# Kernel optimization log

Measured on AMD Instinct MI355X. Metric: run time of the kernel, lower is better.

## Reference

```python
import math
import jax, jax.numpy as jnp
import numpy as np

TREE_DEPTH = 4
NUM_NODES = (1 << TREE_DEPTH) - 1  # 15
TAU_MEM = 0.95
TAU_SYN = 0.95
LN_EPS = 1e-5


def _forward(x, W_proj, threshold, node_weights, gamma, beta):
    B, T, D = x.shape
    padded_T = 1 << math.ceil(math.log2(T))
    x_p = jnp.pad(x, ((0, 0), (0, padded_T - T), (0, 0))) if padded_T > T else x

    eff_depth = min(TREE_DEPTH, int(math.log2(padded_T)))
    num_leaves = 1 << eff_depth
    sub_seq = padded_T // num_leaves
    # leaf states: mean over each contiguous chunk -> [B, num_leaves, D]
    leaves = x_p.reshape(B, num_leaves, sub_seq, D).mean(axis=2)

    leaf_start = (1 << (eff_depth - 1)) - 1
    valid_leaves = min(num_leaves, NUM_NODES - leaf_start)
    node_states = jnp.zeros((B, NUM_NODES, D), x.dtype)
    node_states = node_states.at[:, leaf_start:leaf_start + valid_leaves].set(
        leaves[:, :valid_leaves])

    # LIF membrane/synapse buffers, carried across levels within this forward
    v = jnp.zeros((1, 1, D), x.dtype)
    s = jnp.zeros((1, 1, D), x.dtype)

    # bottom-up tree message passing (static, unrolled: eff_depth levels)
    for level in range(eff_depth - 1, -1, -1):
        level_start = (1 << level) - 1
        level_end = min((1 << (level + 1)) - 1, NUM_NODES)
        nodes = np.arange(level_start, level_end)
        left = 2 * nodes + 1
        right = 2 * nodes + 2
        mask = left < NUM_NODES
        if not mask.any():
            continue  # leaf level: children out of range
        nv, lv, rv = nodes[mask], left[mask], right[mask]
        l_st = node_states[:, lv]   # [B, n, D]
        r_st = node_states[:, rv]   # [B, n, D] (full tree -> rv always valid)
        fused = jnp.concatenate([l_st, r_st], axis=-1)  # [B, n, 2D]
        proj = jnp.einsum('bnk,dk->bnd', fused, W_proj)

        # LIF neuron (training-mode math: surrogate * hard spike)
        s_new = TAU_SYN * s + proj                      # broadcast [B,n,D]
        v_new = TAU_MEM * v + s_new - jax.lax.stop_gradient(s_new)
        spike = (v_new >= threshold).astype(x.dtype)
        v_after = v_new - spike * threshold
        surrogate = jax.nn.sigmoid(25.0 * (v_after - threshold))
        spike_out = surrogate * spike
        v = jax.lax.stop_gradient(v_after.mean(axis=(0, 1), keepdims=True))
        s = jax.lax.stop_gradient(s_new.mean(axis=(0, 1), keepdims=True))

        gated = proj * spike_out
        node_states = node_states.at[:, nv].set(gated)

    # per-dim softmax mixture over the 15 tree nodes
    weights = jax.nn.softmax(node_weights, axis=0)             # [N, D]
    mixture = jnp.einsum('nd,bnd->bd', weights, node_states)   # [B, D]

    out = mixture[:, None, :] + x                              # residual, [B,T,D]
    mu = out.mean(axis=-1, keepdims=True)
    var = out.var(axis=-1, keepdims=True)
    out = (out - mu) / jnp.sqrt(var + LN_EPS) * gamma + beta
    return out


def setup_inputs() -> dict:
    key = jax.random.key(0)
    k0, k1, k2 = jax.random.split(key, 3)
    B, T, D = 8, 4096, 1024
    x = jax.random.normal(k0, (B, T, D), dtype=jnp.float32)
    # nn.Linear(2D, D, bias=False): weight [D, 2D]
    W_proj = jax.random.normal(k1, (D, 2 * D), dtype=jnp.float32) / np.sqrt(2 * D).astype(np.float32)
    threshold = jnp.ones((D,), dtype=jnp.float32)        # LIF init: ones
    node_weights = 0.02 * jax.random.normal(k2, (NUM_NODES, D), dtype=jnp.float32)
    gamma = jnp.ones((D,), dtype=jnp.float32)
    beta = jnp.zeros((D,), dtype=jnp.float32)
    return {"x": x, "W_proj": W_proj, "threshold": threshold,
            "node_weights": node_weights, "gamma": gamma, "beta": beta}


def reference(x, W_proj, threshold, node_weights, gamma, beta):
    return _forward(x, W_proj, threshold, node_weights, gamma, beta)
```

## Files before the change

### kernel.cpp

```cpp
#include <hip/hip_runtime.h>

#define Bq 8
#define Tq 4096
#define Dq 1024
#define NLEAF 8
#define SUBSEQ 256
#define TSPLIT 16
#define NNODES 15

typedef float f32x4 __attribute__((ext_vector_type(4)));

__global__ __launch_bounds__(256) void k_leaf_partial(const float* __restrict__ x,
                                                      float* __restrict__ partial) {
    const int bl = blockIdx.x;
    const int p  = blockIdx.y;
    const int q  = threadIdx.x;
    const int b = bl >> 3, l = bl & 7;
    const float4* xp = (const float4*)(x + ((size_t)b * Tq + (size_t)l * SUBSEQ + (size_t)p * (SUBSEQ / TSPLIT)) * Dq) + q;
    float4 s = {0.f, 0.f, 0.f, 0.f};
#pragma unroll
    for (int t = 0; t < SUBSEQ / TSPLIT; ++t) {
        float4 xv = xp[(size_t)t * (Dq / 4)];
        s.x += xv.x; s.y += xv.y; s.z += xv.z; s.w += xv.w;
    }
    ((float4*)partial)[((size_t)bl * TSPLIT + p) * (Dq / 4) + q] = s;
}

__global__ __launch_bounds__(256) void k_mixture(const float* __restrict__ partial,
                                                 const float* __restrict__ nw,
                                                 float* __restrict__ mixture) {
    const int b = blockIdx.x;
    const int d = blockIdx.y * 256 + threadIdx.x;
    float v[NNODES];
    float m = -1e30f;
#pragma unroll
    for (int n = 0; n < NNODES; ++n) {
        v[n] = nw[n * Dq + d];
        m = fmaxf(m, v[n]);
    }
    float denom = 0.f;
#pragma unroll
    for (int n = 0; n < NNODES; ++n) {
        v[n] = expf(v[n] - m);
        denom += v[n];
    }
    const float inv_denom = 1.0f / denom;
    float acc = 0.f;
#pragma unroll
    for (int l = 0; l < NLEAF; ++l) {
        float s = 0.f;
#pragma unroll
        for (int p = 0; p < TSPLIT; ++p)
            s += partial[(((size_t)(b * NLEAF + l)) * TSPLIT + p) * Dq + d];
        acc += (v[7 + l] * inv_denom) * (s * (1.0f / (float)SUBSEQ));
    }
    mixture[b * Dq + d] = acc;
}

__global__ __launch_bounds__(256) void k_ln(const float* __restrict__ x,
                                            const float* __restrict__ mixture,
                                            const float* __restrict__ gamma,
                                            const float* __restrict__ beta,
                                            float* __restrict__ out) {
    const int wid  = threadIdx.x >> 6;
    const int lane = threadIdx.x & 63;
    const int row  = blockIdx.x * 4 + wid;
    const int b    = row >> 12;
    const float4* xr = (const float4*)(x + (size_t)row * Dq);
    const float4* mr = (const float4*)(mixture + (size_t)b * Dq);
    float4 o[4];
    float sum = 0.f, sq = 0.f;
#pragma unroll
    for (int k = 0; k < 4; ++k) {
        const float4 xv = xr[lane + 64 * k];
        const float4 mv = mr[lane + 64 * k];
        o[k].x = xv.x + mv.x;
        o[k].y = xv.y + mv.y;
        o[k].z = xv.z + mv.z;
        o[k].w = xv.w + mv.w;
        sum += o[k].x + o[k].y + o[k].z + o[k].w;
        sq  += o[k].x * o[k].x + o[k].y * o[k].y + o[k].z * o[k].z + o[k].w * o[k].w;
    }
#pragma unroll
    for (int i = 32; i >= 1; i >>= 1) {
        sum += __shfl_xor(sum, i, 64);
        sq  += __shfl_xor(sq, i, 64);
    }
    const float mu   = sum * (1.0f / 1024.0f);
    const float var  = sq * (1.0f / 1024.0f) - mu * mu;
    const float rstd = rsqrtf(var + 1e-5f);
    f32x4* orow = (f32x4*)(out + (size_t)row * Dq);
#pragma unroll
    for (int k = 0; k < 4; ++k) {
        const float4 gv = ((const float4*)gamma)[lane + 64 * k];
        const float4 bv = ((const float4*)beta)[lane + 64 * k];
        f32x4 r;
        r.x = (o[k].x - mu) * rstd * gv.x + bv.x;
        r.y = (o[k].y - mu) * rstd * gv.y + bv.y;
        r.z = (o[k].z - mu) * rstd * gv.z + bv.z;
        r.w = (o[k].w - mu) * rstd * gv.w + bv.w;
        __builtin_nontemporal_store(r, &orow[lane + 64 * k]);
    }
}

extern "C" void kernel_launch(void* const* d_in, const int* in_sizes, int n_in,
                              void* d_out, int out_size, void* d_ws, size_t ws_size,
                              hipStream_t stream) {
    const float* x     = (const float*)d_in[0];
    const float* nw    = (const float*)d_in[3];
    const float* gamma = (const float*)d_in[4];
    const float* beta  = (const float*)d_in[5];
    float* out = (float*)d_out;

    float* partial = (float*)d_ws;
    float* mixture = partial + (size_t)Bq * NLEAF * TSPLIT * Dq;

    k_leaf_partial<<<dim3(Bq * NLEAF, TSPLIT), 256, 0, stream>>>(x, partial);
    k_mixture<<<dim3(Bq, 4), 256, 0, stream>>>(partial, nw, mixture);
    k_ln<<<Bq * Tq / 4, 256, 0, stream>>>(x, mixture, gamma, beta, out);
}
```

Measured before the change: 61.62 us.

## Fuse leaf chunk reduction and softmax mixture into one column-sliced kernel

Merges the leaf partial-sum kernel and the mixture kernel into a single kernel. Each block owns one batch and a 32-column slice and reduces all 4096 rows in registers, then with shuffles, then through LDS, before applying the softmax-weighted mix. This removes one launch and the round trip through the partial-sum workspace. In exchange it uses only 256 large blocks whose row reads are 128-byte column strips, which may cut memory-level parallelism and coalescing on a bandwidth-bound pass.

```diff
diff --git a/kernel.cpp b/kernel.cpp
--- a/kernel.cpp
+++ b/kernel.cpp
@@ -3,58 +3,88 @@
 #define Bq 8
 #define Tq 4096
 #define Dq 1024
-#define NLEAF 8
-#define SUBSEQ 256
-#define TSPLIT 16
 #define NNODES 15
 
 typedef float f32x4 __attribute__((ext_vector_type(4)));
 
-__global__ __launch_bounds__(256) void k_leaf_partial(const float* __restrict__ x,
-                                                      float* __restrict__ partial) {
-    const int bl = blockIdx.x;
-    const int p  = blockIdx.y;
-    const int q  = threadIdx.x;
-    const int b = bl >> 3, l = bl & 7;
-    const float4* xp = (const float4*)(x + ((size_t)b * Tq + (size_t)l * SUBSEQ + (size_t)p * (SUBSEQ / TSPLIT)) * Dq) + q;
-    float4 s = {0.f, 0.f, 0.f, 0.f};
-#pragma unroll
-    for (int t = 0; t < SUBSEQ / TSPLIT; ++t) {
-        float4 xv = xp[(size_t)t * (Dq / 4)];
-        s.x += xv.x; s.y += xv.y; s.z += xv.z; s.w += xv.w;
-    }
-    ((float4*)partial)[((size_t)bl * TSPLIT + p) * (Dq / 4) + q] = s;
-}
-
-__global__ __launch_bounds__(256) void k_mixture(const float* __restrict__ partial,
+__global__ __launch_bounds__(512) void k_leafmix(const float* __restrict__ x,
                                                  const float* __restrict__ nw,
                                                  float* __restrict__ mixture) {
-    const int b = blockIdx.x;
-    const int d = blockIdx.y * 256 + threadIdx.x;
-    float v[NNODES];
-    float m = -1e30f;
+    const int b     = blockIdx.x >> 5;
+    const int slice = blockIdx.x & 31;
+    const int d0    = slice * 32;
+    const int t     = threadIdx.x;
+    const int qd    = t & 7;
+    const int rg    = t >> 3;
+    const int wv    = t >> 6;
+    const int lane  = t & 63;
+
+    const float4* xb = (const float4*)(x + (size_t)b * Tq * Dq + d0) + qd;
+    float4 acc[8];
 #pragma unroll
-    for (int n = 0; n < NNODES; ++n) {
-        v[n] = nw[n * Dq + d];
-        m = fmaxf(m, v[n]);
+    for (int l = 0; l < 8; ++l) acc[l] = {0.f, 0.f, 0.f, 0.f};
+#pragma unroll
+    for (int l = 0; l < 8; ++l) {
+#pragma unroll
+        for (int j = 0; j < 4; ++j) {
+            const int r = rg + 64 * (l * 4 + j);
+            const float4 xv = xb[(size_t)r * (Dq / 4)];
+            acc[l].x += xv.x; acc[l].y += xv.y;
+            acc[l].z += xv.z; acc[l].w += xv.w;
+        }
     }
-    float denom = 0.f;
 #pragma unroll
-    for (int n = 0; n < NNODES; ++n) {
-        v[n] = expf(v[n] - m);
-        denom += v[n];
+    for (int m = 8; m <= 32; m <<= 1) {
+#pragma unroll
+        for (int l = 0; l < 8; ++l) {
+            acc[l].x += __shfl_xor(acc[l].x, m, 64);
+            acc[l].y += __shfl_xor(acc[l].y, m, 64);
+            acc[l].z += __shfl_xor(acc[l].z, m, 64);
+            acc[l].w += __shfl_xor(acc[l].w, m, 64);
+        }
     }
-    const float inv_denom = 1.0f / denom;
-    float acc = 0.f;
+    __shared__ float4 lds[8][8][8];
+    if (lane < 8) {
 #pragma unroll
-    for (int l = 0; l < NLEAF; ++l) {
-        float s = 0.f;
+        for (int l = 0; l < 8; ++l) lds[wv][lane][l] = acc[l];
+    }
+    __syncthreads();
+    __shared__ float lsum[8][8][4];
+    if (t < 64) {
+        const int q2 = t >> 3, l2 = t & 7;
+        float4 a = lds[0][q2][l2];
 #pragma unroll
-        for (int p = 0; p < TSPLIT; ++p)
-            s += partial[(((size_t)(b * NLEAF + l)) * TSPLIT + p) * Dq + d];
-        acc += (v[7 + l] * inv_denom) * (s * (1.0f / (float)SUBSEQ));
+        for (int w = 1; w < 8; ++w) {
+            a.x += lds[w][q2][l2].x; a.y += lds[w][q2][l2].y;
+            a.z += lds[w][q2][l2].z; a.w += lds[w][q2][l2].w;
+        }
+        lsum[q2][l2][0] = a.x; lsum[q2][l2][1] = a.y;
+        lsum[q2][l2][2] = a.z; lsum[q2][l2][3] = a.w;
     }
-    mixture[b * Dq + d] = acc;
+    __syncthreads();
+    if (t < 32) {
+        const int q2 = t >> 2, c = t & 3;
+        const int d  = d0 + q2 * 4 + c;
+        float v[NNODES];
+        float m = -1e30f;
+#pragma unroll
+        for (int n = 0; n < NNODES; ++n) {
+            v[n] = nw[n * Dq + d];
+            m = fmaxf(m, v[n]);
+        }
+        float denom = 0.f;
+#pragma unroll
+        for (int n = 0; n < NNODES; ++n) {
+            v[n] = expf(v[n] - m);
+            denom += v[n];
+        }
+        const float inv_denom = 1.0f / denom;
+        float mix = 0.f;
+#pragma unroll
+        for (int l = 0; l < 8; ++l)
+            mix += (v[7 + l] * inv_denom) * (lsum[q2][l][c] * (1.0f / 256.0f));
+        mixture[b * Dq + d] = mix;
+    }
 }
 
 __global__ __launch_bounds__(256) void k_ln(const float* __restrict__ x,
@@ -112,10 +142,8 @@
     const float* beta  = (const float*)d_in[5];
     float* out = (float*)d_out;
 
-    float* partial = (float*)d_ws;
-    float* mixture = partial + (size_t)Bq * NLEAF * TSPLIT * Dq;
+    float* mixture = (float*)d_ws;
 
-    k_leaf_partial<<<dim3(Bq * NLEAF, TSPLIT), 256, 0, stream>>>(x, partial);
-    k_mixture<<<dim3(Bq, 4), 256, 0, stream>>>(partial, nw, mixture);
+    k_leafmix<<<Bq * 32, 512, 0, stream>>>(x, nw, mixture);
     k_ln<<<Bq * Tq / 4, 256, 0, stream>>>(x, mixture, gamma, beta, out);
 }
```

New measurement: 56.05 us. 9.0% less time.
